# Performance work log

Hardware: AMD Instinct MI355X
Metric: run time of the kernel (lower is better)

Reference implementation:

```python
import jax, jax.numpy as jnp
import numpy as np

GRAY_THRESHOLD = 127.5  # undefined global in source; midpoint of [0,255] implied by Convert_to_0_255
N_BINS = 512            # 3x3 binary pattern -> codes 0..511
DILATION = 1

# LBP-style fixed conv weights: powers of two laid out row-major
_LBP_W = jnp.array([[256., 128., 64.],
                    [32.,  16.,  8.],
                    [4.,   2.,   1.]], dtype=jnp.float32).reshape(1, 1, 3, 3)  # OIHW


def _pattern_hist(img):
    # img: [N,1,H,W] in [-1,1]-ish range
    x = (img * 0.5 + 0.5) * 255.0          # Convert_to_0_255
    b = (x > GRAY_THRESHOLD).astype(jnp.float32)  # binarize
    # 3x3 valid conv with dilation encodes each 3x3 binary neighborhood as an int code 0..511
    codes = jax.lax.conv_general_dilated(
        b, _LBP_W, window_strides=(1, 1), padding='VALID',
        rhs_dilation=(DILATION, DILATION),
        dimension_numbers=('NCHW', 'OIHW', 'NCHW'))
    idx = codes.reshape(-1).astype(jnp.int32)  # exact integers, int cast == torch .int()
    n = idx.shape[0]
    counts = jnp.zeros((N_BINS,), jnp.float32).at[idx].add(1.0)  # bincount(minlength=512)
    return counts / n


def setup_inputs() -> dict:
    key = jax.random.key(0)
    k1, k2 = jax.random.split(key)
    input = jax.random.normal(k1, (64, 1, 512, 512), dtype=jnp.float32)
    target = jax.random.normal(k2, (64, 1, 512, 512), dtype=jnp.float32)
    return {"input": input, "target": target}


def reference(input, target):
    N, C, H, W = input.shape
    h_in = _pattern_hist(input)
    h_tgt = _pattern_hist(target)
    s = jnp.mean((h_in - h_tgt) ** 2)  # nn.MSELoss
    return s / N / C
```

## Files before the change

### kernel.cpp

```cpp
#include <hip/hip_runtime.h>
#include <stdint.h>

#define HH 512
#define WW 512
#define NIMG 64
#define OH 510
#define OW 510
#define NB 512
#define RPB 16
#define NCHUNK 32
#define NREP 64
#define WAVES 4
#define BLOCK 256

__device__ __forceinline__ int predbit(float x) {
    return ((x * 0.5f + 0.5f) * 255.0f > 127.5f) ? 1 : 0;
}

__global__ __launch_bounds__(BLOCK) void hist_kernel(const float* __restrict__ inp,
                                                     const float* __restrict__ tgt,
                                                     int* __restrict__ rep) {
    __shared__ unsigned long long bits[RPB + 2][9];
    __shared__ int hist[NB];

    const int tid  = threadIdx.x;
    const int lane = tid & 63;
    const int wave = tid >> 6;
    const int chunk = blockIdx.x;
    const int img   = blockIdx.y;
    const int r0 = chunk * RPB;
    const int R  = min(RPB, OH - r0);
    const int rows_in = R + 2;

    for (int i = tid; i < NB; i += BLOCK) hist[i] = 0;

    const float* srcs[2] = {inp, tgt};
    for (int t = 0; t < 2; ++t) {
        const float* src = srcs[t] + (size_t)img * HH * WW + (size_t)r0 * WW;
        __syncthreads();

        const int units = rows_in * 8;
        #pragma unroll 4
        for (int u = wave; u < units; u += WAVES) {
            int row = u >> 3, seg = u & 7;
            float x = src[row * WW + seg * 64 + lane];
            unsigned long long m = __ballot(predbit(x));
            if (lane == 0) bits[row][seg] = m;
        }
        __syncthreads();

        const int sign = 1 - 2 * t;
        const int cmax = min(8, OW - 8 * lane);
        const int word = lane >> 3;
        const int sh   = (8 * lane) & 63;
        for (int o = wave; o < R; o += WAVES) {
            unsigned long long a0 = bits[o][word],     b0 = bits[o][word + 1];
            unsigned long long a1 = bits[o + 1][word], b1 = bits[o + 1][word + 1];
            unsigned long long a2 = bits[o + 2][word], b2 = bits[o + 2][word + 1];
            unsigned long long v0 = (a0 >> sh) | ((b0 << 1) << (63 - sh));
            unsigned long long v1 = (a1 >> sh) | ((b1 << 1) << (63 - sh));
            unsigned long long v2 = (a2 >> sh) | ((b2 << 1) << (63 - sh));
            #pragma unroll
            for (int c = 0; c < 8; ++c) {
                if (c < cmax) {
                    int code = (int)(v0 & 7) | ((int)(v1 & 7) << 3) | ((int)(v2 & 7) << 6);
                    atomicAdd(&hist[code], sign);
                }
                v0 >>= 1; v1 >>= 1; v2 >>= 1;
            }
        }
    }

    __syncthreads();
    const int rid = (blockIdx.y * NCHUNK + blockIdx.x) & (NREP - 1);
    for (int i = tid; i < NB; i += BLOCK) {
        int v = hist[i];
        if (v) atomicAdd(&rep[rid * NB + i], v);
    }
}

__global__ __launch_bounds__(NB) void reduce_kernel(const int* __restrict__ rep,
                                                    float* __restrict__ out) {
    __shared__ double sdata[NB];
    int tid = threadIdx.x;
    int s = 0;
    #pragma unroll
    for (int r = 0; r < NREP; ++r) s += rep[r * NB + tid];
    double d = (double)s;
    sdata[tid] = d * d;
    __syncthreads();
    for (int stp = NB / 2; stp > 0; stp >>= 1) {
        if (tid < stp) sdata[tid] += sdata[tid + stp];
        __syncthreads();
    }
    if (tid == 0) {
        const double n = (double)NIMG * OH * OW;
        out[0] = (float)(sdata[0] / (n * n) / 512.0 / 64.0);
    }
}

extern "C" void kernel_launch(void* const* d_in, const int* in_sizes, int n_in,
                              void* d_out, int out_size, void* d_ws, size_t ws_size,
                              hipStream_t stream) {
    const float* inp = (const float*)d_in[0];
    const float* tgt = (const float*)d_in[1];
    float* out = (float*)d_out;
    int* rep = (int*)d_ws;

    hipMemsetAsync(rep, 0, NREP * NB * sizeof(int), stream);
    hist_kernel<<<dim3(NCHUNK, NIMG), BLOCK, 0, stream>>>(inp, tgt, rep);
    reduce_kernel<<<1, NB, 0, stream>>>(rep, out);
}
```

Measured before the change: 169.4 us.

## Stage both images' bit rows in one pass and reuse rows per wave

The staging phase now loads the input and target tiles together before a single barrier. Each lane issues eight independent global loads before its ballots, so more memory requests are in flight. In the histogram phase each wave owns four consecutive output rows and builds six shifted bit-row words once in registers, instead of rereading three rows from shared memory for every output row. This doubles the shared bit buffer, adds register pressure, and drops a per-image barrier pair in exchange for more memory-level parallelism.

New measurement: 156.6 us. -7.6%, faster.

```diff
diff --git a/kernel.cpp b/kernel.cpp
--- a/kernel.cpp
+++ b/kernel.cpp
@@ -20,7 +20,7 @@
 __global__ __launch_bounds__(BLOCK) void hist_kernel(const float* __restrict__ inp,
                                                      const float* __restrict__ tgt,
                                                      int* __restrict__ rep) {
-    __shared__ unsigned long long bits[RPB + 2][9];
+    __shared__ unsigned long long bits[2][RPB + 2][9];
     __shared__ int hist[NB];
 
     const int tid  = threadIdx.x;
@@ -35,38 +35,52 @@
     for (int i = tid; i < NB; i += BLOCK) hist[i] = 0;
 
     const float* srcs[2] = {inp, tgt};
+    const size_t base = (size_t)img * HH * WW + (size_t)r0 * WW;
+
+    const int nstage = 2 * rows_in;
+    for (int u = wave; u < nstage; u += WAVES) {
+        const int t   = (u >= rows_in) ? 1 : 0;
+        const int row = (u >= rows_in) ? u - rows_in : u;
+        const float* src = srcs[t] + base + (size_t)row * WW + lane;
+        float x[8];
+        #pragma unroll
+        for (int s = 0; s < 8; ++s) x[s] = src[s * 64];
+        unsigned long long m[8];
+        #pragma unroll
+        for (int s = 0; s < 8; ++s) m[s] = __ballot(predbit(x[s]));
+        if (lane == 0) {
+            #pragma unroll
+            for (int s = 0; s < 8; ++s) bits[t][row][s] = m[s];
+        }
+    }
+    __syncthreads();
+
+    const int word = lane >> 3;
+    const int sh   = (8 * lane) & 63;
+    const int cmax = min(8, OW - 8 * lane);
+    const int rbase = wave * 4;
     for (int t = 0; t < 2; ++t) {
-        const float* src = srcs[t] + (size_t)img * HH * WW + (size_t)r0 * WW;
-        __syncthreads();
-
-        const int units = rows_in * 8;
-        #pragma unroll 4
-        for (int u = wave; u < units; u += WAVES) {
-            int row = u >> 3, seg = u & 7;
-            float x = src[row * WW + seg * 64 + lane];
-            unsigned long long m = __ballot(predbit(x));
-            if (lane == 0) bits[row][seg] = m;
+        const int sign = 1 - 2 * t;
+        unsigned long long w[6];
+        #pragma unroll
+        for (int j = 0; j < 6; ++j) {
+            unsigned long long a = bits[t][rbase + j][word];
+            unsigned long long b = bits[t][rbase + j][word + 1];
+            w[j] = (a >> sh) | ((b << 1) << (63 - sh));
         }
-        __syncthreads();
-
-        const int sign = 1 - 2 * t;
-        const int cmax = min(8, OW - 8 * lane);
-        const int word = lane >> 3;
-        const int sh   = (8 * lane) & 63;
-        for (int o = wave; o < R; o += WAVES) {
-            unsigned long long a0 = bits[o][word],     b0 = bits[o][word + 1];
-            unsigned long long a1 = bits[o + 1][word], b1 = bits[o + 1][word + 1];
-            unsigned long long a2 = bits[o + 2][word], b2 = bits[o + 2][word + 1];
-            unsigned long long v0 = (a0 >> sh) | ((b0 << 1) << (63 - sh));
-            unsigned long long v1 = (a1 >> sh) | ((b1 << 1) << (63 - sh));
-            unsigned long long v2 = (a2 >> sh) | ((b2 << 1) << (63 - sh));
-            #pragma unroll
-            for (int c = 0; c < 8; ++c) {
-                if (c < cmax) {
-                    int code = (int)(v0 & 7) | ((int)(v1 & 7) << 3) | ((int)(v2 & 7) << 6);
-                    atomicAdd(&hist[code], sign);
+        #pragma unroll
+        for (int r = 0; r < 4; ++r) {
+            if (rbase + r < R) {
+                unsigned long long v0 = w[r], v1 = w[r + 1], v2 = w[r + 2];
+                #pragma unroll
+                for (int c = 0; c < 8; ++c) {
+                    if (c < cmax) {
+                        int code = (int)((v0 >> c) & 7)
+                                 | ((int)((v1 >> c) & 7) << 3)
+                                 | ((int)((v2 >> c) & 7) << 6);
+                        atomicAdd(&hist[code], sign);
+                    }
                 }
-                v0 >>= 1; v1 >>= 1; v2 >>= 1;
             }
         }
     }
```

## Stream column tiles per wave with rolling ballot masks instead of shared bit buffer

Applied to the files above, without the earlier changes.

Each wave now owns a 62-column by 64-row tile of one image and walks down the rows. It keeps the previous two ballot masks in registers and prefetches four rows ahead, so the shared-memory bit buffer and its two barriers per pass are gone. Each lane emits one code per row and atomically adds it to the shared histogram. Tiles overlap by two columns, so about 3% of input columns are re-read, and each lane now issues one atomic per output pixel instead of eight.

Result: faster. 159.0 us (-6.2%).

```diff
diff --git a/kernel.cpp b/kernel.cpp
--- a/kernel.cpp
+++ b/kernel.cpp
@@ -7,11 +7,12 @@
 #define OH 510
 #define OW 510
 #define NB 512
-#define RPB 16
-#define NCHUNK 32
+#define NTILE 9
+#define NSEG 8
 #define NREP 64
-#define WAVES 4
 #define BLOCK 256
+#define NTASK (NIMG * 2 * NTILE * NSEG)
+#define NBLK (NTASK / 4)
 
 __device__ __forceinline__ int predbit(float x) {
     return ((x * 0.5f + 0.5f) * 255.0f > 127.5f) ? 1 : 0;
@@ -20,59 +21,76 @@
 __global__ __launch_bounds__(BLOCK) void hist_kernel(const float* __restrict__ inp,
                                                      const float* __restrict__ tgt,
                                                      int* __restrict__ rep) {
-    __shared__ unsigned long long bits[RPB + 2][9];
     __shared__ int hist[NB];
-
     const int tid  = threadIdx.x;
     const int lane = tid & 63;
     const int wave = tid >> 6;
-    const int chunk = blockIdx.x;
-    const int img   = blockIdx.y;
-    const int r0 = chunk * RPB;
-    const int R  = min(RPB, OH - r0);
-    const int rows_in = R + 2;
 
     for (int i = tid; i < NB; i += BLOCK) hist[i] = 0;
+    __syncthreads();
 
-    const float* srcs[2] = {inp, tgt};
-    for (int t = 0; t < 2; ++t) {
-        const float* src = srcs[t] + (size_t)img * HH * WW + (size_t)r0 * WW;
-        __syncthreads();
+    const int task = blockIdx.x * 4 + wave;
+    const int seg  = task & (NSEG - 1);
+    const int rst  = task >> 3;
+    const int tile = rst % NTILE;
+    const int rst2 = rst / NTILE;
+    const int t    = rst2 & 1;
+    const int img  = rst2 >> 1;
 
-        const int units = rows_in * 8;
-        #pragma unroll 4
-        for (int u = wave; u < units; u += WAVES) {
-            int row = u >> 3, seg = u & 7;
-            float x = src[row * WW + seg * 64 + lane];
-            unsigned long long m = __ballot(predbit(x));
-            if (lane == 0) bits[row][seg] = m;
-        }
-        __syncthreads();
+    const int r0 = seg * 64;
+    const int R  = min(64, OH - r0);
+    const int colbase = tile * 62;
+    const int col   = min(colbase + lane, WW - 1);
+    const bool valid = (lane < 62) && (colbase + lane < OW);
+    const int sign = 1 - 2 * t;
 
-        const int sign = 1 - 2 * t;
-        const int cmax = min(8, OW - 8 * lane);
-        const int word = lane >> 3;
-        const int sh   = (8 * lane) & 63;
-        for (int o = wave; o < R; o += WAVES) {
-            unsigned long long a0 = bits[o][word],     b0 = bits[o][word + 1];
-            unsigned long long a1 = bits[o + 1][word], b1 = bits[o + 1][word + 1];
-            unsigned long long a2 = bits[o + 2][word], b2 = bits[o + 2][word + 1];
-            unsigned long long v0 = (a0 >> sh) | ((b0 << 1) << (63 - sh));
-            unsigned long long v1 = (a1 >> sh) | ((b1 << 1) << (63 - sh));
-            unsigned long long v2 = (a2 >> sh) | ((b2 << 1) << (63 - sh));
-            #pragma unroll
-            for (int c = 0; c < 8; ++c) {
-                if (c < cmax) {
-                    int code = (int)(v0 & 7) | ((int)(v1 & 7) << 3) | ((int)(v2 & 7) << 6);
-                    atomicAdd(&hist[code], sign);
-                }
-                v0 >>= 1; v1 >>= 1; v2 >>= 1;
-            }
-        }
+    const float* p = (t ? tgt : inp) + (size_t)img * HH * WW + (size_t)r0 * WW + col;
+
+    unsigned long long m0 = __ballot(predbit(p[0]));
+    unsigned long long m1 = __ballot(predbit(p[WW]));
+    float x0 = p[2 * WW], x1 = p[3 * WW], x2 = p[4 * WW], x3 = p[5 * WW];
+
+    int o = 0;
+    for (; o + 4 <= R; o += 4) {
+        {   unsigned long long m2 = __ballot(predbit(x0));
+            int code = (int)((m0 >> lane) & 7) | ((int)((m1 >> lane) & 7) << 3)
+                     | ((int)((m2 >> lane) & 7) << 6);
+            if (valid) atomicAdd(&hist[code], sign);
+            m0 = m1; m1 = m2;
+            int rl = o + 6; if (rl > R + 1) rl = R + 1;
+            x0 = p[rl * WW]; }
+        {   unsigned long long m2 = __ballot(predbit(x1));
+            int code = (int)((m0 >> lane) & 7) | ((int)((m1 >> lane) & 7) << 3)
+                     | ((int)((m2 >> lane) & 7) << 6);
+            if (valid) atomicAdd(&hist[code], sign);
+            m0 = m1; m1 = m2;
+            int rl = o + 7; if (rl > R + 1) rl = R + 1;
+            x1 = p[rl * WW]; }
+        {   unsigned long long m2 = __ballot(predbit(x2));
+            int code = (int)((m0 >> lane) & 7) | ((int)((m1 >> lane) & 7) << 3)
+                     | ((int)((m2 >> lane) & 7) << 6);
+            if (valid) atomicAdd(&hist[code], sign);
+            m0 = m1; m1 = m2;
+            int rl = o + 8; if (rl > R + 1) rl = R + 1;
+            x2 = p[rl * WW]; }
+        {   unsigned long long m2 = __ballot(predbit(x3));
+            int code = (int)((m0 >> lane) & 7) | ((int)((m1 >> lane) & 7) << 3)
+                     | ((int)((m2 >> lane) & 7) << 6);
+            if (valid) atomicAdd(&hist[code], sign);
+            m0 = m1; m1 = m2;
+            int rl = o + 9; if (rl > R + 1) rl = R + 1;
+            x3 = p[rl * WW]; }
+    }
+    for (; o < R; ++o) {
+        unsigned long long m2 = __ballot(predbit(p[(o + 2) * WW]));
+        int code = (int)((m0 >> lane) & 7) | ((int)((m1 >> lane) & 7) << 3)
+                 | ((int)((m2 >> lane) & 7) << 6);
+        if (valid) atomicAdd(&hist[code], sign);
+        m0 = m1; m1 = m2;
     }
 
     __syncthreads();
-    const int rid = (blockIdx.y * NCHUNK + blockIdx.x) & (NREP - 1);
+    const int rid = blockIdx.x & (NREP - 1);
     for (int i = tid; i < NB; i += BLOCK) {
         int v = hist[i];
         if (v) atomicAdd(&rep[rid * NB + i], v);
@@ -108,6 +126,6 @@
     int* rep = (int*)d_ws;
 
     hipMemsetAsync(rep, 0, NREP * NB * sizeof(int), stream);
-    hist_kernel<<<dim3(NCHUNK, NIMG), BLOCK, 0, stream>>>(inp, tgt, rep);
+    hist_kernel<<<NBLK, BLOCK, 0, stream>>>(inp, tgt, rep);
     reduce_kernel<<<1, NB, 0, stream>>>(rep, out);
 }
```

## Restructure LBP histogram into per-wave column tiles with pipelined vector loads

Applied to the files above, without the earlier changes.

Replaces the ballot-to-shared-bitmask scheme with per-wave tasks, each covering a 256-column tile and 16 output rows. Each lane loads float4 per row through an 8-deep register ring of inline-asm global loads with manual vmcnt waits, builds nibbles and neighbor bits via a shuffle, and emits codes directly to the shared histogram. The two codes per row that straddle the tile seam are handled by separate seam tasks, and out-of-range lanes write to padding bins instead of branching. The block-wide barriers between the load and count phases go away, and there is more memory-level parallelism per wave. In exchange the code carries fragile hand-written waitcnt sequencing and a threshold rewritten as x > 2^-24.

After: 151.2 us. 1.12x faster.

```diff
diff --git a/kernel.cpp b/kernel.cpp
--- a/kernel.cpp
+++ b/kernel.cpp
@@ -7,75 +7,129 @@
 #define OH 510
 #define OW 510
 #define NB 512
-#define RPB 16
-#define NCHUNK 32
+#define SEGR 16
+#define NSEG 32
 #define NREP 64
-#define WAVES 4
 #define BLOCK 256
+#define NBIG (NIMG * 2 * NSEG * 2)
+#define NSEAM (NIMG * 2 * 8)
+#define NBLK ((NBIG + NSEAM) / 4)
+#define HBINS 576
 
-__device__ __forceinline__ int predbit(float x) {
-    return ((x * 0.5f + 0.5f) * 255.0f > 127.5f) ? 1 : 0;
+typedef float f4 __attribute__((ext_vector_type(4)));
+
+__device__ __forceinline__ f4 ldg4(const float* addr) {
+    f4 r;
+    asm volatile("global_load_dwordx4 %0, %1, off" : "=v"(r) : "v"(addr));
+    return r;
+}
+template<int N>
+__device__ __forceinline__ void waitv(f4& x) {
+    if      constexpr (N == 7) asm volatile("s_waitcnt vmcnt(7)" : "+v"(x));
+    else if constexpr (N == 6) asm volatile("s_waitcnt vmcnt(6)" : "+v"(x));
+    else if constexpr (N == 5) asm volatile("s_waitcnt vmcnt(5)" : "+v"(x));
+    else if constexpr (N == 4) asm volatile("s_waitcnt vmcnt(4)" : "+v"(x));
+    else if constexpr (N == 3) asm volatile("s_waitcnt vmcnt(3)" : "+v"(x));
+    else if constexpr (N == 2) asm volatile("s_waitcnt vmcnt(2)" : "+v"(x));
+    else if constexpr (N == 1) asm volatile("s_waitcnt vmcnt(1)" : "+v"(x));
+    else                       asm volatile("s_waitcnt vmcnt(0)" : "+v"(x));
+}
+
+#define BINC 0x1p-24f
+
+__device__ __forceinline__ int pack4(f4 v) {
+    return (v.x > BINC) | ((v.y > BINC) << 1) | ((v.z > BINC) << 2) | ((v.w > BINC) << 3);
 }
 
 __global__ __launch_bounds__(BLOCK) void hist_kernel(const float* __restrict__ inp,
                                                      const float* __restrict__ tgt,
                                                      int* __restrict__ rep) {
-    __shared__ unsigned long long bits[RPB + 2][9];
-    __shared__ int hist[NB];
-
+    __shared__ int hist[HBINS];
     const int tid  = threadIdx.x;
     const int lane = tid & 63;
     const int wave = tid >> 6;
-    const int chunk = blockIdx.x;
-    const int img   = blockIdx.y;
-    const int r0 = chunk * RPB;
-    const int R  = min(RPB, OH - r0);
-    const int rows_in = R + 2;
 
-    for (int i = tid; i < NB; i += BLOCK) hist[i] = 0;
+    for (int i = tid; i < HBINS; i += BLOCK) hist[i] = 0;
+    __syncthreads();
 
-    const float* srcs[2] = {inp, tgt};
-    for (int t = 0; t < 2; ++t) {
-        const float* src = srcs[t] + (size_t)img * HH * WW + (size_t)r0 * WW;
-        __syncthreads();
+    const int task  = blockIdx.x * 4 + wave;
+    const int dummy = 512 + lane;
 
-        const int units = rows_in * 8;
-        #pragma unroll 4
-        for (int u = wave; u < units; u += WAVES) {
-            int row = u >> 3, seg = u & 7;
-            float x = src[row * WW + seg * 64 + lane];
-            unsigned long long m = __ballot(predbit(x));
-            if (lane == 0) bits[row][seg] = m;
+    if (task < NBIG) {
+        const int tile = task & 1;
+        const int seg  = (task >> 1) & 31;
+        const int t    = (task >> 6) & 1;
+        const int img  = task >> 7;
+        const int r0   = seg * SEGR;
+        const int R    = min(SEGR, OH - r0);
+        const int c0   = tile * 256 + 4 * lane;
+        const int sign = 1 - 2 * t;
+        const float* base = (t ? tgt : inp) + (size_t)img * (HH * WW) + c0;
+        auto ap = [&](int rel) { return base + (size_t)min(r0 + rel, HH - 1) * WW; };
+
+        f4 X[8];
+        #pragma unroll
+        for (int k = 0; k < 8; ++k) X[k] = ldg4(ap(k));
+
+        int n0, n1, n2;
+        waitv<7>(X[0]);
+        { int nib = pack4(X[0]); n0 = nib | (__shfl_down(nib, 1) << 4); }
+        X[0] = ldg4(ap(8));
+        waitv<7>(X[1]);
+        { int nib = pack4(X[1]); n1 = nib | (__shfl_down(nib, 1) << 4); }
+        X[1] = ldg4(ap(9));
+
+        #define STEP(o, W) { \
+            f4& Xs = X[((o) + 2) & 7]; \
+            waitv<W>(Xs); \
+            int nib = pack4(Xs); \
+            n2 = nib | (__shfl_down(nib, 1) << 4); \
+            if ((o) <= 7) Xs = ldg4(ap((o) + 10)); \
+            if ((o) < R) { \
+                _Pragma("unroll") \
+                for (int j = 0; j < 4; ++j) { \
+                    int code = ((n0 >> j) & 7) | (((n1 >> j) & 7) << 3) \
+                             | (((n2 >> j) & 7) << 6); \
+                    int slot = (lane < 63 || j < 2) ? code : dummy; \
+                    atomicAdd(&hist[slot], sign); \
+                } \
+            } \
+            n0 = n1; n1 = n2; }
+
+        STEP(0, 7)  STEP(1, 7)  STEP(2, 7)  STEP(3, 7)
+        STEP(4, 7)  STEP(5, 7)  STEP(6, 7)  STEP(7, 7)
+        STEP(8, 7)  STEP(9, 6)  STEP(10, 5) STEP(11, 4)
+        STEP(12, 3) STEP(13, 2) STEP(14, 1) STEP(15, 0)
+        #undef STEP
+    } else {
+        const int idx = task - NBIG;
+        const int seg = idx & 7;
+        const int t   = (idx >> 3) & 1;
+        const int img = idx >> 4;
+        const int sign = 1 - 2 * t;
+        const int r   = seg * 64 + lane;
+        const bool v  = (r < OH);
+        const float* bp = (t ? tgt : inp) + (size_t)img * (HH * WW);
+        int p[3];
+        #pragma unroll
+        for (int k = 0; k < 3; ++k) {
+            const float* rowp = bp + (size_t)min(r + k, HH - 1) * WW;
+            float2 A = *(const float2*)(rowp + 254);
+            float2 B = *(const float2*)(rowp + 256);
+            p[k] = (A.x > BINC) | ((A.y > BINC) << 1)
+                 | ((B.x > BINC) << 2) | ((B.y > BINC) << 3);
         }
-        __syncthreads();
-
-        const int sign = 1 - 2 * t;
-        const int cmax = min(8, OW - 8 * lane);
-        const int word = lane >> 3;
-        const int sh   = (8 * lane) & 63;
-        for (int o = wave; o < R; o += WAVES) {
-            unsigned long long a0 = bits[o][word],     b0 = bits[o][word + 1];
-            unsigned long long a1 = bits[o + 1][word], b1 = bits[o + 1][word + 1];
-            unsigned long long a2 = bits[o + 2][word], b2 = bits[o + 2][word + 1];
-            unsigned long long v0 = (a0 >> sh) | ((b0 << 1) << (63 - sh));
-            unsigned long long v1 = (a1 >> sh) | ((b1 << 1) << (63 - sh));
-            unsigned long long v2 = (a2 >> sh) | ((b2 << 1) << (63 - sh));
-            #pragma unroll
-            for (int c = 0; c < 8; ++c) {
-                if (c < cmax) {
-                    int code = (int)(v0 & 7) | ((int)(v1 & 7) << 3) | ((int)(v2 & 7) << 6);
-                    atomicAdd(&hist[code], sign);
-                }
-                v0 >>= 1; v1 >>= 1; v2 >>= 1;
-            }
-        }
+        int c254 = (p[0] & 7) | ((p[1] & 7) << 3) | ((p[2] & 7) << 6);
+        int c255 = ((p[0] >> 1) & 7) | (((p[1] >> 1) & 7) << 3) | (((p[2] >> 1) & 7) << 6);
+        atomicAdd(&hist[v ? c254 : dummy], sign);
+        atomicAdd(&hist[v ? c255 : dummy], sign);
     }
 
     __syncthreads();
-    const int rid = (blockIdx.y * NCHUNK + blockIdx.x) & (NREP - 1);
+    const int rid = blockIdx.x & (NREP - 1);
     for (int i = tid; i < NB; i += BLOCK) {
-        int v = hist[i];
-        if (v) atomicAdd(&rep[rid * NB + i], v);
+        int vv = hist[i];
+        if (vv) atomicAdd(&rep[rid * NB + i], vv);
     }
 }
 
@@ -108,6 +162,6 @@
     int* rep = (int*)d_ws;
 
     hipMemsetAsync(rep, 0, NREP * NB * sizeof(int), stream);
-    hist_kernel<<<dim3(NCHUNK, NIMG), BLOCK, 0, stream>>>(inp, tgt, rep);
+    hist_kernel<<<NBLK, BLOCK, 0, stream>>>(inp, tgt, rep);
     reduce_kernel<<<1, NB, 0, stream>>>(rep, out);
 }
```
